# Optimization experiments

Measured on AMD Instinct MI355X. Metric: run time of the kernel, lower is better.

The kernel has to match this reference:

```python
import jax, jax.numpy as jnp
import numpy as np

B, C, H, W, K = 32, 384, 56, 56, 7
EPS = 1e-6


def setup_inputs() -> dict:
    key = jax.random.key(0)
    ks = jax.random.split(key, 8)
    return {
        "x": jax.random.normal(ks[0], (B, C, H, W), dtype=jnp.float32),
        "w_avg": jax.random.normal(ks[1], (C, C), dtype=jnp.float32) * 0.05,
        "b_avg": jax.random.normal(ks[2], (C,), dtype=jnp.float32) * 0.05,
        "w_max": jax.random.normal(ks[3], (C, C), dtype=jnp.float32) * 0.05,
        "b_max": jax.random.normal(ks[4], (C,), dtype=jnp.float32) * 0.05,
        "w_mix": jax.random.normal(ks[5], (C, K * K), dtype=jnp.float32) * 0.05,
        "gamma": jax.random.normal(ks[6], (C, 1, 1), dtype=jnp.float32),
        "beta": jax.random.normal(ks[7], (C, 1, 1), dtype=jnp.float32),
    }


def reference(x, w_avg, b_avg, w_max, b_max, w_mix, gamma, beta):
    b, c, h, w = x.shape
    k = int(np.sqrt(w_mix.shape[1]))
    pad = k // 2

    # dual pooling -> 1x1 convs (pure channel matmuls) -> GELU (exact, torch default)
    x_avg = x.mean(axis=(2, 3))                      # [B, C]
    x_max = x.max(axis=(2, 3))                       # [B, C]
    x_w = jax.nn.gelu(
        x_avg @ w_avg.T + b_avg + x_max @ w_max.T + b_max, approximate=False
    )                                                # [B, C]

    # conv_mix: grouped 1x1 conv, groups=C, 1 in-ch per group, k*k out-ch per group
    x_w = x_w[:, :, None] * w_mix[None, :, :]        # [B, C, K*K]

    # FGRN: filter-wise global response normalization
    xr = x_w.reshape(b, c, k, k)
    Gx = jnp.sqrt(jnp.sum(xr * xr, axis=(2, 3), keepdims=True))   # [B, C, 1, 1]
    Nx = Gx / (Gx.mean(axis=1, keepdims=True) + EPS)
    kern = gamma[None] * (xr * Nx) + beta[None]      # [B, C, K, K]

    # per-sample dynamic depthwise conv via grouped-conv trick
    x_flat = x.reshape(1, b * c, h, w)
    w_flat = kern.reshape(b * c, 1, k, k)
    out = jax.lax.conv_general_dilated(
        x_flat, w_flat,
        window_strides=(1, 1),
        padding=[(pad, pad), (pad, pad)],
        feature_group_count=b * c,
        dimension_numbers=("NCHW", "OIHW", "NCHW"),
    )
    return out.reshape(b, c, h, w)
```

## Files before the change

### kernel.cpp

```cpp
#include <hip/hip_runtime.h>
#include <math.h>

#define BB 32
#define CC 384
#define HH 56
#define WW 56
#define HWSZ (HH*WW)
#define EPSF 1e-6f

typedef float float2v __attribute__((ext_vector_type(2)));

__device__ __forceinline__ float dpp_shr1(float v) {
    return __int_as_float(__builtin_amdgcn_update_dpp(
        0, __float_as_int(v), 0x111, 0xF, 0xF, true));
}
__device__ __forceinline__ float dpp_shl1(float v) {
    return __int_as_float(__builtin_amdgcn_update_dpp(
        0, __float_as_int(v), 0x101, 0xF, 0xF, true));
}

__global__ __launch_bounds__(256) void pool_kernel(const float* __restrict__ x,
                                                   float* __restrict__ xavg,
                                                   float* __restrict__ xmax) {
    int plane = blockIdx.x;
    const float4* xp = (const float4*)(x + (size_t)plane * HWSZ);
    int t = threadIdx.x;
    float s = 0.f, m = -INFINITY;
    for (int i = t; i < HWSZ/4; i += 256) {
        float4 v = xp[i];
        s += v.x + v.y + v.z + v.w;
        m = fmaxf(m, fmaxf(fmaxf(v.x, v.y), fmaxf(v.z, v.w)));
    }
    for (int off = 32; off; off >>= 1) {
        s += __shfl_down(s, off, 64);
        m = fmaxf(m, __shfl_down(m, off, 64));
    }
    __shared__ float ss[4], sm[4];
    int wid = t >> 6;
    if ((t & 63) == 0) { ss[wid] = s; sm[wid] = m; }
    __syncthreads();
    if (t == 0) {
        s = ss[0] + ss[1] + ss[2] + ss[3];
        m = fmaxf(fmaxf(sm[0], sm[1]), fmaxf(sm[2], sm[3]));
        xavg[plane] = s * (1.0f / HWSZ);
        xmax[plane] = m;
    }
}

__global__ __launch_bounds__(256) void gemv_kernel(
        const float* __restrict__ xavg, const float* __restrict__ xmax,
        const float* __restrict__ w_avg, const float* __restrict__ b_avg,
        const float* __restrict__ w_max, const float* __restrict__ b_max,
        const float* __restrict__ w_mix,
        float* __restrict__ xw, float* __restrict__ Gx, float* __restrict__ partG) {
    int blk = blockIdx.x;
    int b  = blk / 6;
    int cg = blk - b*6;
    int t  = threadIdx.x;
    int ch = cg*64 + (t >> 2);
    int kl = t & 3;

    const float4* wa = (const float4*)(w_avg + (size_t)ch * CC) + kl*24;
    const float4* wm = (const float4*)(w_max + (size_t)ch * CC) + kl*24;
    const float4* xa = (const float4*)(xavg + (size_t)b * CC) + kl*24;
    const float4* xm = (const float4*)(xmax + (size_t)b * CC) + kl*24;

    float acc = 0.f;
    #pragma unroll 4
    for (int q = 0; q < 24; ++q) {
        float4 a4 = wa[q], v4 = xa[q];
        acc += a4.x*v4.x + a4.y*v4.y + a4.z*v4.z + a4.w*v4.w;
    }
    #pragma unroll 4
    for (int q = 0; q < 24; ++q) {
        float4 m4 = wm[q], v4 = xm[q];
        acc += m4.x*v4.x + m4.y*v4.y + m4.z*v4.z + m4.w*v4.w;
    }
    acc += __shfl_xor(acc, 1);
    acc += __shfl_xor(acc, 2);

    float val = acc + b_avg[ch] + b_max[ch];
    float xwv = 0.5f * val * (1.0f + erff(val * 0.70710678118654752f));

    float sq = 0.f;
    const float* wr = w_mix + (size_t)ch * 49;
    #pragma unroll
    for (int i = 0; i < 13; ++i) {
        int j = kl + 4*i;
        if (j < 49) { float v = wr[j]; sq += v*v; }
    }
    sq += __shfl_xor(sq, 1);
    sq += __shfl_xor(sq, 2);
    float Gxv = fabsf(xwv) * sqrtf(sq);

    __shared__ float sg[64];
    if (kl == 0) {
        xw[b*CC + ch] = xwv;
        Gx[b*CC + ch] = Gxv;
        sg[t >> 2] = Gxv;
    }
    __syncthreads();
    if (t < 64) {
        float v = sg[t];
        for (int off = 32; off; off >>= 1) v += __shfl_down(v, off, 64);
        if (t == 0) partG[blk] = v;
    }
}

__global__ __launch_bounds__(128) void conv_kernel(const float* __restrict__ x,
                                                   const float* __restrict__ xw,
                                                   const float* __restrict__ Gx,
                                                   const float* __restrict__ partG,
                                                   const float* __restrict__ w_mix,
                                                   const float* __restrict__ gamma,
                                                   const float* __restrict__ beta,
                                                   float* __restrict__ out) {
    int t = threadIdx.x;
    int plane = blockIdx.x;
    const float4* xp4 = (const float4*)(x + (size_t)plane * HWSZ);
    float4* op4 = (float4*)(out + (size_t)plane * HWSZ);

    float kfv[49];
    {
        int b = plane / CC;
        int c = plane - b*CC;
        float sG = partG[b*6+0] + partG[b*6+1] + partG[b*6+2]
                 + partG[b*6+3] + partG[b*6+4] + partG[b*6+5];
        float xwv = xw[plane];
        float Gxv = Gx[plane];
        float gam = gamma[c];
        float bet = beta[c];
        float coef = gam * xwv * (Gxv / (sG * (1.0f/CC) + EPSF));
        const float* wr = w_mix + (size_t)c * 49;
        #pragma unroll
        for (int j = 0; j < 49; ++j) {
            union { float f; int i; } u;
            u.f = coef * wr[j] + bet;
            u.i = __builtin_amdgcn_readfirstlane(u.i);
            kfv[j] = u.f;
        }
    }

    int s = t & 15;
    int g = (t >> 4) & 7;
    bool active = (s < 14);
    int sc = active ? s : 13;
    int g7 = 7*g - 3;

    float2v acc2[7][2];
    #pragma unroll
    for (int i = 0; i < 7; ++i) {
        acc2[i][0] = (float2v){0.f, 0.f};
        acc2[i][1] = (float2v){0.f, 0.f};
    }

    float4 z4 = make_float4(0.f, 0.f, 0.f, 0.f);

    #pragma unroll
    for (int ry = 0; ry < 13; ++ry) {
        int ri = g7 + ry;
        int ric = min(max(ri, 0), 55);
        float4 vb = xp4[ric*14 + sc];
        bool ok = ((unsigned)ri < 56u) && active;
        if (!ok) vb = z4;

        float w0 = dpp_shr1(vb.y);
        float w1 = dpp_shr1(vb.z);
        float w2 = dpp_shr1(vb.w);
        float w7 = dpp_shl1(vb.x);
        float w8 = dpp_shl1(vb.y);
        float w9 = dpp_shl1(vb.z);

        float2v wp[5], wq[4];
        wp[0] = (float2v){w0,   w1};
        wp[1] = (float2v){w2,   vb.x};
        wp[2] = (float2v){vb.y, vb.z};
        wp[3] = (float2v){vb.w, w7};
        wp[4] = (float2v){w8,   w9};
        wq[0] = (float2v){w1,   w2};
        wq[1] = (float2v){vb.x, vb.y};
        wq[2] = (float2v){vb.z, vb.w};
        wq[3] = (float2v){w7,   w8};

        int oy_lo = (ry - 6 > 0) ? (ry - 6) : 0;
        int oy_hi = (ry < 6) ? ry : 6;
        #pragma unroll
        for (int oy = 0; oy < 7; ++oy) {
            if (oy < oy_lo || oy > oy_hi) continue;
            int ky = ry - oy;
            #pragma unroll
            for (int kx = 0; kx < 7; ++kx) {
                float kv = kfv[ky*7 + kx];
                float2v kv2 = {kv, kv};
                float2v pa = (kx & 1) ? wq[kx >> 1]       : wp[kx >> 1];
                float2v pb = (kx & 1) ? wq[(kx >> 1) + 1] : wp[(kx >> 1) + 1];
                acc2[oy][0] = __builtin_elementwise_fma(kv2, pa, acc2[oy][0]);
                acc2[oy][1] = __builtin_elementwise_fma(kv2, pb, acc2[oy][1]);
            }
        }
    }

    if (active) {
        #pragma unroll
        for (int oy = 0; oy < 7; ++oy) {
            int orow = 7*g + oy;
            float4 o;
            o.x = acc2[oy][0].x; o.y = acc2[oy][0].y;
            o.z = acc2[oy][1].x; o.w = acc2[oy][1].y;
            op4[orow*14 + sc] = o;
        }
    }
}

extern "C" void kernel_launch(void* const* d_in, const int* in_sizes, int n_in,
                              void* d_out, int out_size, void* d_ws, size_t ws_size,
                              hipStream_t stream) {
    const float* x     = (const float*)d_in[0];
    const float* w_avg = (const float*)d_in[1];
    const float* b_avg = (const float*)d_in[2];
    const float* w_max = (const float*)d_in[3];
    const float* b_max = (const float*)d_in[4];
    const float* w_mix = (const float*)d_in[5];
    const float* gamma = (const float*)d_in[6];
    const float* beta  = (const float*)d_in[7];
    float* out = (float*)d_out;

    float* ws    = (float*)d_ws;
    float* xavg  = ws;
    float* xmax  = ws + BB*CC;
    float* xwbuf = ws + 2*BB*CC;
    float* Gxbuf = ws + 3*BB*CC;
    float* partG = ws + 4*BB*CC;

    pool_kernel<<<BB*CC, 256, 0, stream>>>(x, xavg, xmax);
    gemv_kernel<<<BB*6, 256, 0, stream>>>(xavg, xmax, w_avg, b_avg, w_max, b_max,
                                          w_mix, xwbuf, Gxbuf, partG);
    conv_kernel<<<BB*CC, 128, 0, stream>>>(x, xwbuf, Gxbuf, partG, w_mix, gamma, beta, out);
}
```

Measured before the change: 98.42 us.

## Precompute conv taps in separate kernel and prefetch input rows in conv

Result: no change. 100.3 us (+1.9%).

```diff
diff --git a/kernel.cpp b/kernel.cpp
--- a/kernel.cpp
+++ b/kernel.cpp
@@ -107,39 +107,34 @@
     }
 }
 
+__global__ __launch_bounds__(256) void taps_kernel(
+        const float* __restrict__ xw, const float* __restrict__ Gx,
+        const float* __restrict__ partG, const float* __restrict__ w_mix,
+        const float* __restrict__ gamma, const float* __restrict__ beta,
+        float* __restrict__ kern) {
+    int plane = blockIdx.x * 256 + threadIdx.x;
+    int b = plane / CC;
+    int c = plane - b*CC;
+    float sG = partG[b*6+0] + partG[b*6+1] + partG[b*6+2]
+             + partG[b*6+3] + partG[b*6+4] + partG[b*6+5];
+    float xwv = xw[plane];
+    float Gxv = Gx[plane];
+    float coef = gamma[c] * xwv * (Gxv / (sG * (1.0f/CC) + EPSF));
+    float bet  = beta[c];
+    const float* wr = w_mix + (size_t)c * 49;
+    float* kp = kern + (size_t)plane * 49;
+    #pragma unroll
+    for (int j = 0; j < 49; ++j) kp[j] = coef * wr[j] + bet;
+}
+
 __global__ __launch_bounds__(128) void conv_kernel(const float* __restrict__ x,
-                                                   const float* __restrict__ xw,
-                                                   const float* __restrict__ Gx,
-                                                   const float* __restrict__ partG,
-                                                   const float* __restrict__ w_mix,
-                                                   const float* __restrict__ gamma,
-                                                   const float* __restrict__ beta,
+                                                   const float* __restrict__ kern,
                                                    float* __restrict__ out) {
     int t = threadIdx.x;
+    int lane = t & 63;
     int plane = blockIdx.x;
     const float4* xp4 = (const float4*)(x + (size_t)plane * HWSZ);
     float4* op4 = (float4*)(out + (size_t)plane * HWSZ);
-
-    float kfv[49];
-    {
-        int b = plane / CC;
-        int c = plane - b*CC;
-        float sG = partG[b*6+0] + partG[b*6+1] + partG[b*6+2]
-                 + partG[b*6+3] + partG[b*6+4] + partG[b*6+5];
-        float xwv = xw[plane];
-        float Gxv = Gx[plane];
-        float gam = gamma[c];
-        float bet = beta[c];
-        float coef = gam * xwv * (Gxv / (sG * (1.0f/CC) + EPSF));
-        const float* wr = w_mix + (size_t)c * 49;
-        #pragma unroll
-        for (int j = 0; j < 49; ++j) {
-            union { float f; int i; } u;
-            u.f = coef * wr[j] + bet;
-            u.i = __builtin_amdgcn_readfirstlane(u.i);
-            kfv[j] = u.f;
-        }
-    }
 
     int s = t & 15;
     int g = (t >> 4) & 7;
@@ -147,6 +142,21 @@
     int sc = active ? s : 13;
     int g7 = 7*g - 3;
 
+    float kv_lane = kern[(size_t)plane * 49 + lane];
+
+    float4 pf[13];
+    #pragma unroll
+    for (int i = 0; i < 4; ++i) {
+        int ri = g7 + i;
+        int ric = min(max(ri, 0), 55);
+        pf[i] = xp4[ric*14 + sc];
+    }
+
+    float kfv[49];
+    #pragma unroll
+    for (int j = 0; j < 49; ++j)
+        kfv[j] = __int_as_float(__builtin_amdgcn_readlane(__float_as_int(kv_lane), j));
+
     float2v acc2[7][2];
     #pragma unroll
     for (int i = 0; i < 7; ++i) {
@@ -158,11 +168,15 @@
 
     #pragma unroll
     for (int ry = 0; ry < 13; ++ry) {
+        if (ry + 4 < 13) {
+            int ri = g7 + ry + 4;
+            int ric = min(max(ri, 0), 55);
+            pf[ry + 4] = xp4[ric*14 + sc];
+        }
+
         int ri = g7 + ry;
-        int ric = min(max(ri, 0), 55);
-        float4 vb = xp4[ric*14 + sc];
         bool ok = ((unsigned)ri < 56u) && active;
-        if (!ok) vb = z4;
+        float4 vb = ok ? pf[ry] : z4;
 
         float w0 = dpp_shr1(vb.y);
         float w1 = dpp_shr1(vb.z);
@@ -231,9 +245,11 @@
     float* xwbuf = ws + 2*BB*CC;
     float* Gxbuf = ws + 3*BB*CC;
     float* partG = ws + 4*BB*CC;
+    float* kern  = ws + 4*BB*CC + 256;
 
     pool_kernel<<<BB*CC, 256, 0, stream>>>(x, xavg, xmax);
     gemv_kernel<<<BB*6, 256, 0, stream>>>(xavg, xmax, w_avg, b_avg, w_max, b_max,
                                           w_mix, xwbuf, Gxbuf, partG);
-    conv_kernel<<<BB*CC, 128, 0, stream>>>(x, xwbuf, Gxbuf, partG, w_mix, gamma, beta, out);
-}
+    taps_kernel<<<BB*CC/256, 256, 0, stream>>>(xwbuf, Gxbuf, partG, w_mix, gamma, beta, kern);
+    conv_kernel<<<BB*CC, 128, 0, stream>>>(x, kern, out);
+}
```
